# Optimization experiments

Hardware: AMD Instinct MI355X
Metric: run time of the kernel (lower is better)

The kernel has to match this reference:

```python
import jax, jax.numpy as jnp
import numpy as np

N, D, H, N_HEADS = 2048, 512, 512, 16

def setup_inputs() -> dict:
    key = jax.random.key(0)
    k1, k2, k3 = jax.random.split(key, 3)
    inputs = jax.random.normal(k1, (N, D), dtype=jnp.float32)
    idx = jax.random.randint(k2, (N,), 0, N_HEADS, dtype=jnp.int64)
    weights = jax.random.normal(k3, (N_HEADS, D, H), dtype=jnp.float32)
    biases = jnp.zeros((N_HEADS, H), dtype=jnp.float32)
    return {"inputs": inputs, "idx": idx, "weights": weights, "biases": biases}

def reference(inputs, idx, weights, biases):
    # per-sample weight gather: (N, D, H) then batched vec-mat: (N, 1, D) @ (N, D, H) -> (N, H)
    w = weights[idx]            # (N, D, H)  -- the redundant materialized gather
    b = biases[idx]             # (N, H)
    return jnp.einsum('nd,ndh->nh', inputs, w) + b
```

## Files before the change

kernel.cpp:

```cpp
#include <hip/hip_runtime.h>


#define N_SAMPLES 2048
#define DIM       512
#define HDIM      512
#define N_HEADS   16
#define SH        16
#define BPITCH    520

typedef __attribute__((ext_vector_type(8))) short bf16x8;
typedef __attribute__((ext_vector_type(4))) float floatx4;

__device__ inline unsigned short f2bf_rne(float f) {
    union { float f; unsigned u; } v; v.f = f;
    return (unsigned short)((v.u + 0x7FFFu + ((v.u >> 16) & 1u)) >> 16);
}

__device__ inline unsigned bf2_trunc(float lo, float hi) {
    return __builtin_amdgcn_perm(__float_as_uint(hi), __float_as_uint(lo), 0x07060302u);
}

__device__ inline bf16x8 pack_a(const float4 u0, const float4 u1) {
    union { bf16x8 v; unsigned u[4]; } r;
    r.u[0] = bf2_trunc(u0.x, u0.y);
    r.u[1] = bf2_trunc(u0.z, u0.w);
    r.u[2] = bf2_trunc(u1.x, u1.y);
    r.u[3] = bf2_trunc(u1.z, u1.w);
    return r.v;
}

__global__ __launch_bounds__(256, 2) void fused(
    const float* __restrict__ x,
    const int*   __restrict__ idx,
    const float* __restrict__ w,
    const float* __restrict__ bias,
    float*       __restrict__ out)
{
    __shared__ unsigned short Bl[SH * BPITCH];
    __shared__ int slist[N_SAMPLES];
    __shared__ int wcnt[4];

    const int bid  = blockIdx.x;
    const int head = bid >> 5;
    const int h0   = (bid & 31) * SH;
    const int t    = threadIdx.x;
    const int wave = t >> 6;
    const int lane = t & 63;
    const int l16  = lane & 15;
    const int quad = lane >> 4;

    {
        const float* wg = w + (size_t)head * DIM * HDIM + h0;
        #pragma unroll
        for (int i = 0; i < 8; ++i) {
            const int flat = i * 256 + t;
            const int d    = flat >> 2;
            const int hg   = (flat & 3) * 4;
            const float4 v = *(const float4*)(wg + (size_t)d * HDIM + hg);
            Bl[(hg + 0) * BPITCH + d] = f2bf_rne(v.x);
            Bl[(hg + 1) * BPITCH + d] = f2bf_rne(v.y);
            Bl[(hg + 2) * BPITCH + d] = f2bf_rne(v.z);
            Bl[(hg + 3) * BPITCH + d] = f2bf_rne(v.w);
        }
    }

    unsigned long long masks[8];
    {
        int mycnt = 0;
        #pragma unroll
        for (int c = 0; c < 8; ++c) {
            const int n = (wave * 8 + c) * 64 + lane;
            masks[c] = __ballot(idx[n] == head);
            mycnt += __popcll(masks[c]);
        }
        if (lane == 0) wcnt[wave] = mycnt;
    }
    __syncthreads();
    int cnt = 0, base = 0;
    #pragma unroll
    for (int i = 0; i < 4; ++i) { if (i < wave) base += wcnt[i]; cnt += wcnt[i]; }
    {
        int pos = base;
        #pragma unroll
        for (int c = 0; c < 8; ++c) {
            const unsigned long long m = masks[c];
            if (m & (1ull << lane)) {
                const int rank = __popcll(m & ((1ull << lane) - 1ull));
                slist[pos + rank] = (wave * 8 + c) * 64 + lane;
            }
            pos += __popcll(m);
        }
    }
    __syncthreads();

    const float bv = bias[head * HDIM + h0 + l16];

    for (int p = wave; p * 32 < cnt; p += 4) {
        const int t0 = 2 * p, t1 = 2 * p + 1;
        const int mg0 = t0 * 16 + l16;
        const int mg1 = t1 * 16 + l16;
        const int r0 = slist[mg0 < cnt ? mg0 : cnt - 1];
        const int r1 = slist[mg1 < cnt ? mg1 : cnt - 1];
        const float* xp0 = x + (size_t)r0 * DIM + quad * 8;
        const float* xp1 = x + (size_t)r1 * DIM + quad * 8;

        bf16x8 a0[16], a1[16];
        #pragma unroll
        for (int ks = 0; ks < 16; ++ks) {
            const float4 u0 = *(const float4*)(xp0 + ks * 32);
            const float4 u1 = *(const float4*)(xp0 + ks * 32 + 4);
            const float4 v0 = *(const float4*)(xp1 + ks * 32);
            const float4 v1 = *(const float4*)(xp1 + ks * 32 + 4);
            a0[ks] = pack_a(u0, u1);
            a1[ks] = pack_a(v0, v1);
        }

        floatx4 acc0 = {0.f, 0.f, 0.f, 0.f};
        floatx4 acc1 = {0.f, 0.f, 0.f, 0.f};
        #pragma unroll
        for (int ks = 0; ks < 16; ++ks) {
            const bf16x8 bfrag = *(const bf16x8*)&Bl[l16 * BPITCH + ks * 32 + quad * 8];
            acc0 = __builtin_amdgcn_mfma_f32_16x16x32_bf16(a0[ks], bfrag, acc0, 0, 0, 0);
            acc1 = __builtin_amdgcn_mfma_f32_16x16x32_bf16(a1[ks], bfrag, acc1, 0, 0, 0);
        }

        #pragma unroll
        for (int r = 0; r < 4; ++r) {
            const int m0 = t0 * 16 + quad * 4 + r;
            if (m0 < cnt) out[(size_t)slist[m0] * HDIM + h0 + l16] = acc0[r] + bv;
            const int m1 = t1 * 16 + quad * 4 + r;
            if (m1 < cnt) out[(size_t)slist[m1] * HDIM + h0 + l16] = acc1[r] + bv;
        }
    }
}

extern "C" void kernel_launch(void* const* d_in, const int* in_sizes, int n_in,
                              void* d_out, int out_size, void* d_ws, size_t ws_size,
                              hipStream_t stream) {
    const float* x   = (const float*)d_in[0];
    const int*   idx = (const int*)  d_in[1];
    const float* w   = (const float*)d_in[2];
    const float* b   = (const float*)d_in[3];
    float*       out = (float*)d_out;

    fused<<<N_HEADS * (HDIM / SH), 256, 0, stream>>>(x, idx, w, b, out);
}
```

Before: 94.60 us.

## Split each head/column tile across two blocks and raise occupancy

```diff
diff --git a/kernel.cpp b/kernel.cpp
--- a/kernel.cpp
+++ b/kernel.cpp
@@ -6,6 +6,7 @@
 #define HDIM      512
 #define N_HEADS   16
 #define SH        16
+#define SG        2
 #define BPITCH    520
 
 typedef __attribute__((ext_vector_type(8))) short bf16x8;
@@ -15,11 +16,12 @@
     union { float f; unsigned u; } v; v.f = f;
     return (unsigned short)((v.u + 0x7FFFu + ((v.u >> 16) & 1u)) >> 16);
 }
-
+__device__ inline unsigned bfpack_rne(float lo, float hi) {
+    return (unsigned)f2bf_rne(lo) | ((unsigned)f2bf_rne(hi) << 16);
+}
 __device__ inline unsigned bf2_trunc(float lo, float hi) {
     return __builtin_amdgcn_perm(__float_as_uint(hi), __float_as_uint(lo), 0x07060302u);
 }
-
 __device__ inline bf16x8 pack_a(const float4 u0, const float4 u1) {
     union { bf16x8 v; unsigned u[4]; } r;
     r.u[0] = bf2_trunc(u0.x, u0.y);
@@ -29,7 +31,7 @@
     return r.v;
 }
 
-__global__ __launch_bounds__(256, 2) void fused(
+__global__ __launch_bounds__(256, 4) void fused(
     const float* __restrict__ x,
     const int*   __restrict__ idx,
     const float* __restrict__ w,
@@ -41,26 +43,34 @@
     __shared__ int wcnt[4];
 
     const int bid  = blockIdx.x;
-    const int head = bid >> 5;
-    const int h0   = (bid & 31) * SH;
+    const int sg   = bid & (SG - 1);
+    const int sid  = bid >> 1;
+    const int head = sid >> 5;
+    const int h0   = (sid & 31) * SH;
     const int t    = threadIdx.x;
     const int wave = t >> 6;
     const int lane = t & 63;
     const int l16  = lane & 15;
     const int quad = lane >> 4;
 
+    int myidx[8];
+    #pragma unroll
+    for (int c = 0; c < 8; ++c)
+        myidx[c] = idx[(wave * 8 + c) * 64 + lane];
+
     {
         const float* wg = w + (size_t)head * DIM * HDIM + h0;
         #pragma unroll
-        for (int i = 0; i < 8; ++i) {
+        for (int i = 0; i < 4; ++i) {
             const int flat = i * 256 + t;
-            const int d    = flat >> 2;
+            const int dp   = flat >> 2;
             const int hg   = (flat & 3) * 4;
-            const float4 v = *(const float4*)(wg + (size_t)d * HDIM + hg);
-            Bl[(hg + 0) * BPITCH + d] = f2bf_rne(v.x);
-            Bl[(hg + 1) * BPITCH + d] = f2bf_rne(v.y);
-            Bl[(hg + 2) * BPITCH + d] = f2bf_rne(v.z);
-            Bl[(hg + 3) * BPITCH + d] = f2bf_rne(v.w);
+            const float4 v0 = *(const float4*)(wg + (size_t)(2 * dp) * HDIM + hg);
+            const float4 v1 = *(const float4*)(wg + (size_t)(2 * dp + 1) * HDIM + hg);
+            *(unsigned*)&Bl[(hg + 0) * BPITCH + 2 * dp] = bfpack_rne(v0.x, v1.x);
+            *(unsigned*)&Bl[(hg + 1) * BPITCH + 2 * dp] = bfpack_rne(v0.y, v1.y);
+            *(unsigned*)&Bl[(hg + 2) * BPITCH + 2 * dp] = bfpack_rne(v0.z, v1.z);
+            *(unsigned*)&Bl[(hg + 3) * BPITCH + 2 * dp] = bfpack_rne(v0.w, v1.w);
         }
     }
 
@@ -69,8 +79,7 @@
         int mycnt = 0;
         #pragma unroll
         for (int c = 0; c < 8; ++c) {
-            const int n = (wave * 8 + c) * 64 + lane;
-            masks[c] = __ballot(idx[n] == head);
+            masks[c] = __ballot(myidx[c] == head);
             mycnt += __popcll(masks[c]);
         }
         if (lane == 0) wcnt[wave] = mycnt;
@@ -95,7 +104,7 @@
 
     const float bv = bias[head * HDIM + h0 + l16];
 
-    for (int p = wave; p * 32 < cnt; p += 4) {
+    for (int p = wave + 4 * sg; p * 32 < cnt; p += 4 * SG) {
         const int t0 = 2 * p, t1 = 2 * p + 1;
         const int mg0 = t0 * 16 + l16;
         const int mg1 = t1 * 16 + l16;
@@ -104,24 +113,17 @@
         const float* xp0 = x + (size_t)r0 * DIM + quad * 8;
         const float* xp1 = x + (size_t)r1 * DIM + quad * 8;
 
-        bf16x8 a0[16], a1[16];
+        floatx4 acc0 = {0.f, 0.f, 0.f, 0.f};
+        floatx4 acc1 = {0.f, 0.f, 0.f, 0.f};
         #pragma unroll
         for (int ks = 0; ks < 16; ++ks) {
             const float4 u0 = *(const float4*)(xp0 + ks * 32);
             const float4 u1 = *(const float4*)(xp0 + ks * 32 + 4);
             const float4 v0 = *(const float4*)(xp1 + ks * 32);
             const float4 v1 = *(const float4*)(xp1 + ks * 32 + 4);
-            a0[ks] = pack_a(u0, u1);
-            a1[ks] = pack_a(v0, v1);
-        }
-
-        floatx4 acc0 = {0.f, 0.f, 0.f, 0.f};
-        floatx4 acc1 = {0.f, 0.f, 0.f, 0.f};
-        #pragma unroll
-        for (int ks = 0; ks < 16; ++ks) {
             const bf16x8 bfrag = *(const bf16x8*)&Bl[l16 * BPITCH + ks * 32 + quad * 8];
-            acc0 = __builtin_amdgcn_mfma_f32_16x16x32_bf16(a0[ks], bfrag, acc0, 0, 0, 0);
-            acc1 = __builtin_amdgcn_mfma_f32_16x16x32_bf16(a1[ks], bfrag, acc1, 0, 0, 0);
+            acc0 = __builtin_amdgcn_mfma_f32_16x16x32_bf16(pack_a(u0, u1), bfrag, acc0, 0, 0, 0);
+            acc1 = __builtin_amdgcn_mfma_f32_16x16x32_bf16(pack_a(v0, v1), bfrag, acc1, 0, 0, 0);
         }
 
         #pragma unroll
@@ -143,5 +145,5 @@
     const float* b   = (const float*)d_in[3];
     float*       out = (float*)d_out;
 
-    fused<<<N_HEADS * (HDIM / SH), 256, 0, stream>>>(x, idx, w, b, out);
+    fused<<<N_HEADS * (HDIM / SH) * SG, 256, 0, stream>>>(x, idx, w, b, out);
 }
```

After: 108.5 us. 14.7% more time.
